# Kernel optimization log

Measured on AMD Instinct MI355X. Metric: run time of the kernel, lower is better.

The kernel has to match this reference:

```python
import jax, jax.numpy as jnp
import numpy as np

N_ANCHORS = 262144
N_GT = 100
IMG = 1024.0
N_SAMPLE = 256
POS_RATIO = 0.5
POS_T = 0.7
NEG_T = 0.3
ALLOWED_BORDER = 0.0
NUM_FG = int(POS_RATIO * N_SAMPLE)  # 128


def compute_overlap(a, g):
    """IoU between anchors a:(N,4) and gt g:(R,4), py-faster-rcnn +1 pixel convention."""
    area_a = (a[:, 2] - a[:, 0] + 1.0) * (a[:, 3] - a[:, 1] + 1.0)          # (N,)
    area_g = (g[:, 2] - g[:, 0] + 1.0) * (g[:, 3] - g[:, 1] + 1.0)          # (R,)
    iw = jnp.minimum(a[:, None, 2], g[None, :, 2]) - jnp.maximum(a[:, None, 0], g[None, :, 0]) + 1.0
    ih = jnp.minimum(a[:, None, 3], g[None, :, 3]) - jnp.maximum(a[:, None, 1], g[None, :, 1]) + 1.0
    inter = jnp.maximum(iw, 0.0) * jnp.maximum(ih, 0.0)                     # (N,R)
    return inter / (area_a[:, None] + area_g[None, :] - inter)


def bbox_transform(gt, an):
    """Encode gt boxes relative to anchors -> (dx,dy,dw,dh), shape (N,4)."""
    aw = an[:, 2] - an[:, 0] + 1.0
    ah = an[:, 3] - an[:, 1] + 1.0
    acx = an[:, 0] + 0.5 * aw
    acy = an[:, 1] + 0.5 * ah
    gw = gt[:, 2] - gt[:, 0] + 1.0
    gh = gt[:, 3] - gt[:, 1] + 1.0
    gcx = gt[:, 0] + 0.5 * gw
    gcy = gt[:, 1] + 0.5 * gh
    return jnp.stack([(gcx - acx) / aw, (gcy - acy) / ah,
                      jnp.log(gw / aw), jnp.log(gh / ah)], axis=1)


def keep_at_most(mask, k, key):
    """Keep at most k True entries of mask, chosen uniformly at random (fixed shape)."""
    r = jnp.where(mask, jax.random.uniform(key, mask.shape), jnp.inf)
    rank = jnp.argsort(jnp.argsort(r))  # rank[i] = position of i in ascending sort
    return mask & (rank < k)


def anchor_target(anchors, image_shape, gt, key):
    # anchors: (N,4), gt: (R,4)
    R = gt.shape[0]
    inside = ((anchors[:, 0] >= -ALLOWED_BORDER) & (anchors[:, 1] >= -ALLOWED_BORDER)
              & (anchors[:, 2] < ALLOWED_BORDER + image_shape[1])
              & (anchors[:, 3] < ALLOWED_BORDER + image_shape[0]))            # (N,)
    iou = compute_overlap(anchors, gt)                                        # (N,R)
    iou_m = jnp.where(inside[:, None], iou, -1.0)  # restrict to inside anchors
    max_ov = jnp.max(iou_m, axis=1)                                           # (N,)

    k1, k2, k3 = jax.random.split(key, 3)
    labels = jnp.full(anchors.shape[:1], -1.0, dtype=jnp.float32)
    # clobber_positives=False: background first
    labels = jnp.where(inside & (max_ov < NEG_T), 0.0, labels)
    # per-gt argmax anchors (tie set), randomly truncated to at most R like tf.random_shuffle[:R]
    gt_max = jnp.max(iou_m, axis=0)                                           # (R,)
    cand = jnp.any(iou_m == gt_max[None, :], axis=1) & inside                 # (N,)
    cand = keep_at_most(cand, R, k1)
    labels = jnp.where(cand, 1.0, labels)
    labels = jnp.where(inside & (max_ov >= POS_T), 1.0, labels)

    # balance: subsample positives to NUM_FG
    fg = labels == 1.0
    labels = jnp.where(fg & ~keep_at_most(fg, NUM_FG, k2), -1.0, labels)
    # subsample negatives to n_sample - n_fg
    n_fg = jnp.sum(labels == 1.0)
    bg = labels == 0.0
    labels = jnp.where(bg & ~keep_at_most(bg, N_SAMPLE - n_fg, k3), -1.0, labels)
    # umap: outside anchors stay -1
    labels = jnp.where(inside, labels, -1.0)

    # bbox targets: faithful to original tf.gather(gt, to_int32(max_overlaps))
    idx = jnp.clip(max_ov.astype(jnp.int32), 0, R - 1)
    tgt = bbox_transform(gt[idx], anchors)                                    # (N,4)
    tgt = jnp.where(inside[:, None], tgt, 0.0)  # scatter_nd at inside indices
    return labels[None], tgt[None]


def setup_inputs() -> dict:
    key = jax.random.key(0)
    k1, k2, k3, k4 = jax.random.split(key, 4)
    ctr = jax.random.uniform(k1, (N_ANCHORS, 2), minval=-64.0, maxval=IMG + 64.0)
    wh = jax.random.uniform(k2, (N_ANCHORS, 2), minval=16.0, maxval=256.0)
    anchors = jnp.concatenate([ctr - 0.5 * wh, ctr + 0.5 * wh], axis=1)
    gctr = jax.random.uniform(k3, (N_GT, 2), minval=100.0, maxval=IMG - 100.0)
    gwh = jax.random.uniform(k4, (N_GT, 2), minval=30.0, maxval=200.0)
    gt = jnp.concatenate([gctr - 0.5 * gwh, gctr + 0.5 * gwh], axis=1)
    return {"total_anchors": anchors[None],
            "image_shape": jnp.array([IMG, IMG], jnp.float32),
            "gt_boxes": gt[None]}


def reference(total_anchors, image_shape, gt_boxes):
    key = jax.random.key(42)  # original uses unseeded tf.random_shuffle
    labels, bbox_reg_targets = anchor_target(total_anchors[0], image_shape,
                                             gt_boxes[0][:, :4], key)
    return labels, bbox_reg_targets
```

## Files before the change

### kernel.cpp

```cpp
#include <hip/hip_runtime.h>
#include <stdint.h>

#define NGT_MAX 128
#define CAND_CAP 8192
#define CSEL_CAP 512
#define FILT_CAP 16384
#define SUB_CAP 2048


__host__ __device__ inline void tf2x32(uint32_t k0, uint32_t k1, uint32_t c0, uint32_t c1,
                                       uint32_t& o0, uint32_t& o1) {
  uint32_t ks[3] = {k0, k1, k0 ^ k1 ^ 0x1BD11BDAu};
  uint32_t x0 = c0 + ks[0];
  uint32_t x1 = c1 + ks[1];
  const int rot[2][4] = {{13, 15, 26, 6}, {17, 29, 16, 24}};
#pragma unroll
  for (int i = 0; i < 5; ++i) {
#pragma unroll
    for (int j = 0; j < 4; ++j) {
      x0 += x1;
      int r = rot[i & 1][j];
      x1 = (x1 << r) | (x1 >> (32 - r));
      x1 ^= x0;
    }
    x0 += ks[(i + 1) % 3];
    x1 += ks[(i + 2) % 3] + (uint32_t)(i + 1);
  }
  o0 = x0; o1 = x1;
}

__device__ inline uint64_t sel_key(uint32_t i, uint32_t ka, uint32_t kb) {
  uint32_t o0, o1;
  tf2x32(ka, kb, 0u, i, o0, o1);
  uint32_t bits = o0 ^ o1;
  return ((uint64_t)(bits >> 9) << 32) | (uint64_t)i;
}

__device__ inline uint32_t fmap(float v) {
  uint32_t u = __float_as_uint(v);
  return (u & 0x80000000u) ? ~u : (u | 0x80000000u);
}
__device__ inline float funmap(uint32_t m) {
  return (m & 0x80000000u) ? __uint_as_float(m & 0x7FFFFFFFu) : __uint_as_float(~m);
}

__device__ inline void cons_meta(uint32_t baseF, uint32_t baseB, uint32_t* needF,
                                 uint32_t* Tf, uint32_t* needB, uint32_t* Tb) {
  *needF = (baseF > 128u) ? 1u : 0u;
  uint64_t tf = 0, tb = 0;
  if (*needF) {
    tf = (((uint64_t)(128u * 32u)) << 23) / (uint64_t)baseF;
    if (tf > (1u << 23)) tf = (1u << 23);
  }
  uint32_t nfgmin = baseF < 128u ? baseF : 128u;
  uint32_t kbgmax = 256u - nfgmin;
  *needB = (baseB > 8192u + kbgmax) ? 1u : 0u;
  if (*needB) {
    tb = (((uint64_t)(kbgmax * 32u)) << 23) / (uint64_t)(baseB - 8192u);
    if (tb > (1u << 23)) tb = (1u << 23);
  }
  *Tf = (uint32_t)tf;
  *Tb = (uint32_t)tb;
}

__global__ void __launch_bounds__(256)
k_main(const float4* __restrict__ anc, const float* __restrict__ img,
       const float4* __restrict__ gt, int N, int R,
       uint32_t* __restrict__ pmax, uint32_t* __restrict__ gmaxu,
       float* __restrict__ LBL, float4* __restrict__ TGT,
       uint32_t* __restrict__ pmeta, uint32_t* __restrict__ counters) {
  __shared__ float4 sgt[NGT_MAX];
  __shared__ float sarea[NGT_MAX];
  __shared__ float sq[64 * 101];
  __shared__ uint32_t scnt[2];
  const int t = threadIdx.x, b = blockIdx.x;
  if (b == 0 && t < 16) counters[t] = 0u;
  if (t < 2) scnt[t] = 0u;
  if (t < R) {
    float4 g = gt[t];
    sgt[t] = g;
    {
#pragma clang fp contract(off)
      sarea[t] = (g.z - g.x + 1.0f) * (g.w - g.y + 1.0f);
    }
  }
  __syncthreads();
  const int lane = t & 63, lm = t & 3, q = t >> 2;
  const int i = b * 256 + t;
  const float H = img[0], W = img[1];
  float4 a = anc[i];
  bool inside = (a.x >= 0.0f) && (a.y >= 0.0f) && (a.z < W) && (a.w < H);
  float area_a;
  {
#pragma clang fp contract(off)
    area_a = (a.z - a.x + 1.0f) * (a.w - a.y + 1.0f);
  }
  if (!inside) area_a = __uint_as_float(0x7FC00000u);
  const bool b1 = (lm == 1), b2 = (lm == 2), b3 = (lm == 3);
  float part[25];
  float vmax = -1.0f;
#pragma unroll 4
  for (int s = 0; s < 25; ++s) {
    const int gb0 = 4 * s;
    if (gb0 >= R) break;
    float v2q[4];
#pragma unroll
    for (int k = 0; k < 4; ++k) {
      const int g = gb0 + k;
      if (g < R) {
        float4 gb = sgt[g];
        float v;
        {
#pragma clang fp contract(off)
          float iw = fminf(a.z, gb.z) - fmaxf(a.x, gb.x) + 1.0f;
          float ih = fminf(a.w, gb.w) - fmaxf(a.y, gb.y) + 1.0f;
          float inter = fmaxf(iw, 0.0f) * fmaxf(ih, 0.0f);
          v = inter / (area_a + sarea[g] - inter);
        }
        vmax = fmaxf(vmax, v);
        int s1 = __builtin_amdgcn_mov_dpp(__float_as_int(v), 0xB1, 0xF, 0xF, true);
        float v1 = fmaxf(v, __int_as_float(s1));
        int s2 = __builtin_amdgcn_mov_dpp(__float_as_int(v1), 0x4E, 0xF, 0xF, true);
        v2q[k] = fmaxf(v1, __int_as_float(s2));
      } else {
        v2q[k] = -1.0f;
      }
    }
    float p = v2q[0];
    p = b1 ? v2q[1] : p;
    p = b2 ? v2q[2] : p;
    p = b3 ? v2q[3] : p;
    part[s] = p;
  }
  float lbl = -1.0f;
  if (inside) {
    if (vmax < 0.3f) lbl = 0.0f;
    if (vmax >= 0.7f) lbl = 1.0f;
  }
  LBL[i] = lbl;
  unsigned long long bf = __ballot(lbl == 1.0f);
  unsigned long long bb = __ballot(lbl == 0.0f);
  if (lane == 0) {
    atomicAdd(&scnt[0], (uint32_t)__popcll(bf));
    atomicAdd(&scnt[1], (uint32_t)__popcll(bb));
  }
  float4 o = make_float4(0.f, 0.f, 0.f, 0.f);
  if (inside) {
    int idx = (int)vmax;
    idx = idx < 0 ? 0 : (idx > R - 1 ? R - 1 : idx);
    float4 gb = sgt[idx];
    {
#pragma clang fp contract(off)
      float aw = a.z - a.x + 1.0f;
      float ah = a.w - a.y + 1.0f;
      float acx = a.x + 0.5f * aw;
      float acy = a.y + 0.5f * ah;
      float gw = gb.z - gb.x + 1.0f;
      float gh = gb.w - gb.y + 1.0f;
      float gcx = gb.x + 0.5f * gw;
      float gcy = gb.y + 0.5f * gh;
      o.x = (gcx - acx) / aw;
      o.y = (gcy - acy) / ah;
      o.z = logf(gw / aw);
      o.w = logf(gh / ah);
    }
  }
  TGT[i] = o;
#pragma unroll
  for (int s = 0; s < 25; ++s) {
    const int g = 4 * s + lm;
    if (4 * s >= R) break;
    if (g < R) sq[q * 101 + g] = part[s];
  }
  __syncthreads();
  if (t < R) {
    float m = -1.0f;
#pragma unroll 8
    for (int k2 = 0; k2 < 64; ++k2) m = fmaxf(m, sq[k2 * 101 + t]);
    uint32_t u = fmap(m);
    pmax[b * R + t] = u;
    if (u > gmaxu[t]) atomicMax(&gmaxu[t], u);
  }
  if (t == 0) pmeta[b] = scnt[0] | (scnt[1] << 16);
}

__global__ void __launch_bounds__(256)
k_gather(const float4* __restrict__ anc, const float* __restrict__ img,
         const float4* __restrict__ gt, int N, int NB, int R,
         const uint32_t* __restrict__ pmax, const uint32_t* __restrict__ gmaxu,
         const uint32_t* __restrict__ pmeta,
         float* __restrict__ LBL,
         uint64_t* __restrict__ candList, uint32_t* __restrict__ candLbl,
         uint64_t* __restrict__ listF, uint64_t* __restrict__ listB,
         uint32_t* __restrict__ counters,
         uint32_t k1a, uint32_t k1b, uint32_t k2a, uint32_t k2b,
         uint32_t k3a, uint32_t k3b) {
  __shared__ uint64_t red[256];
  __shared__ int tg[NGT_MAX];
  __shared__ float tgm[NGT_MAX];
  __shared__ uint64_t cbuf[256];
  __shared__ uint32_t cbufL[256];
  __shared__ uint64_t bufF[256], bufB[256];
  __shared__ uint32_t cC, cF, cB, oC, oF, oB;
  __shared__ int tcnt;
  const int t = threadIdx.x, b = blockIdx.x;
  if (t == 0) { tcnt = 0; cC = 0u; cF = 0u; cB = 0u; }
  uint64_t sm = 0;
  for (int j = t; j < NB; j += 256) {
    uint32_t v = pmeta[j];
    sm += (uint64_t)(v & 0xFFFFu) | ((uint64_t)(v >> 16) << 32);
  }
  red[t] = sm;
  __syncthreads();
  for (int s = 128; s > 0; s >>= 1) {
    if (t < s) red[t] += red[t + s];
    __syncthreads();
  }
  const uint32_t baseF = (uint32_t)(red[0] & 0xFFFFFFFFu);
  const uint32_t baseB = (uint32_t)(red[0] >> 32);
  uint32_t needF, Tf, needB, Tb;
  cons_meta(baseF, baseB, &needF, &Tf, &needB, &Tb);
  if (t < R) {
    uint32_t pm = pmax[b * R + t];
    uint32_t gm = gmaxu[t];
    if (pm == gm) { int p = atomicAdd(&tcnt, 1); tg[p] = t; tgm[p] = funmap(gm); }
  }
  __syncthreads();
  const int C0 = tcnt;
  const int i = b * 256 + t;
  float old = LBL[i];
  bool isc = false;
  if (C0 > 0) {
    const float H = img[0], W = img[1];
    float4 a = anc[i];
    bool inside = (a.x >= 0.0f) && (a.y >= 0.0f) && (a.z < W) && (a.w < H);
    if (inside) {
      float area_a;
      {
#pragma clang fp contract(off)
        area_a = (a.z - a.x + 1.0f) * (a.w - a.y + 1.0f);
      }
      for (int j = 0; j < C0; ++j) {
        float4 gb = gt[tg[j]];
        float v;
        {
#pragma clang fp contract(off)
          float ag = (gb.z - gb.x + 1.0f) * (gb.w - gb.y + 1.0f);
          float iw = fminf(a.z, gb.z) - fmaxf(a.x, gb.x) + 1.0f;
          float ih = fminf(a.w, gb.w) - fmaxf(a.y, gb.y) + 1.0f;
          float inter = fmaxf(iw, 0.0f) * fmaxf(ih, 0.0f);
          v = inter / (area_a + ag - inter);
        }
        isc = isc || (v == tgm[j]);
      }
    }
  }
  if (isc) {
    uint32_t code = (old == 1.0f) ? 2u : ((old == 0.0f) ? 1u : 0u);
    uint32_t p = atomicAdd(&cC, 1u);
    cbuf[p] = sel_key((uint32_t)i, k1a, k1b);
    cbufL[p] = code;
  }
  float l1 = isc ? 1.0f : old;
  float out = l1;
  if (l1 == 1.0f) {
    uint64_t key = sel_key((uint32_t)i, k2a, k2b);
    if (needF && (uint32_t)(key >> 32) >= Tf) {
      out = -1.0f;
    } else {
      uint32_t p = atomicAdd(&cF, 1u);
      bufF[p] = key;
    }
  } else if (l1 == 0.0f) {
    uint64_t key = sel_key((uint32_t)i, k3a, k3b);
    if (needB && (uint32_t)(key >> 32) >= Tb) {
      out = -1.0f;
    } else {
      uint32_t p = atomicAdd(&cB, 1u);
      bufB[p] = key;
    }
  }
  LBL[i] = out;
  __syncthreads();
  if (t == 0 && cC) oC = atomicAdd(&counters[0], cC);
  if (t == 64 && cF) oF = atomicAdd(&counters[4], cF);
  if (t == 128 && cB) oB = atomicAdd(&counters[5], cB);
  __syncthreads();
  for (uint32_t j = t; j < cC; j += 256) {
    uint32_t p = oC + j;
    if (p < CAND_CAP) { candList[p] = cbuf[j]; candLbl[p] = cbufL[j]; }
  }
  for (uint32_t j = t; j < cF; j += 256) {
    uint32_t p = oF + j;
    if (p < FILT_CAP) listF[p] = bufF[j];
  }
  for (uint32_t j = t; j < cB; j += 256) {
    uint32_t p = oB + j;
    if (p < FILT_CAP) listB[p] = bufB[j];
  }
}

__device__ __forceinline__ void do_select(const uint64_t* list, uint32_t Mf, uint32_t k,
                                          uint32_t T, float* LBL, uint32_t* h,
                                          uint32_t* c0, uint32_t* c1, uint64_t* sub,
                                          uint32_t* scal, const uint32_t* drop,
                                          uint32_t nd) {
  const int t = threadIdx.x;
  if (Mf <= k) return;
  int bl = (T > 1u) ? (32 - __clz(T - 1u)) : 0;
  int shift = bl > 8 ? bl - 8 : 0;
  h[t] = 0u;
  if (t == 0) { scal[0] = 0u; scal[1] = 0u; scal[2] = 0u; }
  __syncthreads();
  for (uint32_t j = t; j < Mf; j += 256) {
    uint64_t key = list[j];
    bool skip = false;
    for (uint32_t d = 0; d < nd; ++d) skip = skip || (drop[d] == (uint32_t)key);
    if (!skip) atomicAdd(&h[((uint32_t)(key >> 32)) >> shift], 1u);
  }
  __syncthreads();
  c0[t] = h[t];
  __syncthreads();
  uint32_t* s = c0;
  uint32_t* d2 = c1;
  for (int dd = 1; dd < 256; dd <<= 1) {
    uint32_t v = s[t];
    if (t >= dd) v += s[t - dd];
    d2[t] = v;
    __syncthreads();
    uint32_t* tmp = s; s = d2; d2 = tmp;
  }
  uint32_t inc = s[t];
  uint32_t exc = inc - h[t];
  if (exc < k && inc >= k) { scal[1] = (uint32_t)t; scal[2] = k - exc; }
  __syncthreads();
  const uint32_t binb = scal[1], rneed = scal[2];
  for (uint32_t j = t; j < Mf; j += 256) {
    uint64_t key = list[j];
    bool skip = false;
    for (uint32_t d = 0; d < nd; ++d) skip = skip || (drop[d] == (uint32_t)key);
    if (skip) continue;
    uint32_t bin = ((uint32_t)(key >> 32)) >> shift;
    if (bin > binb) {
      LBL[(uint32_t)key] = -1.0f;
    } else if (bin == binb) {
      uint32_t p = atomicAdd(&scal[0], 1u);
      if (p < SUB_CAP) sub[p] = key;
    }
  }
  __syncthreads();
  uint32_t c = scal[0] < SUB_CAP ? scal[0] : SUB_CAP;
  for (uint32_t s2 = t; s2 < c; s2 += 256) {
    uint64_t key = sub[s2];
    uint32_t rank = 0u;
    for (uint32_t j = 0; j < c; ++j) rank += (sub[j] < key) ? 1u : 0u;
    if (rank >= rneed) LBL[(uint32_t)key] = -1.0f;
  }
  __syncthreads();
}

__global__ void __launch_bounds__(256)
k_sel(float* __restrict__ LBL, uint64_t* __restrict__ listF,
      uint64_t* __restrict__ listB, const uint64_t* __restrict__ candList,
      const uint32_t* __restrict__ candLbl, const uint32_t* __restrict__ pmeta,
      uint32_t* __restrict__ counters, int NB, int R,
      uint32_t k3a, uint32_t k3b) {
  __shared__ uint64_t red[256];
  __shared__ uint64_t ck[CSEL_CAP];
  __shared__ uint32_t cc[CSEL_CAP];
  __shared__ uint32_t drop[256];
  __shared__ uint32_t h[256], c0s[256], c1s[256];
  __shared__ uint64_t sub[SUB_CAP];
  __shared__ uint32_t scal[8];
  const int t = threadIdx.x;
  uint64_t sm = 0;
  for (int j = t; j < NB; j += 256) {
    uint32_t v = pmeta[j];
    sm += (uint64_t)(v & 0xFFFFu) | ((uint64_t)(v >> 16) << 32);
  }
  red[t] = sm;
  if (t < 8) scal[t] = 0u;
  uint32_t C = counters[0];
  if (C > CSEL_CAP) C = CSEL_CAP;
  for (uint32_t s = t; s < C; s += 256) { ck[s] = candList[s]; cc[s] = candLbl[s]; }
  __syncthreads();
  for (int s = 128; s > 0; s >>= 1) {
    if (t < s) red[t] += red[t + s];
    __syncthreads();
  }
  const uint32_t baseF = (uint32_t)(red[0] & 0xFFFFFFFFu);
  const uint32_t baseB = (uint32_t)(red[0] >> 32);
  uint32_t needFc, TfC, needBc, TbC;
  cons_meta(baseF, baseB, &needFc, &TfC, &needBc, &TbC);
  const uint32_t MfB0 = counters[5] < FILT_CAP ? counters[5] : FILT_CAP;
  for (uint32_t e = t; e < C; e += 256) {
    uint64_t key = ck[e];
    bool keep = true;
    if (C > (uint32_t)R) {
      uint32_t rank = 0;
      for (uint32_t j = 0; j < C; ++j) rank += (ck[j] < key) ? 1u : 0u;
      keep = (rank < (uint32_t)R);
    }
    uint32_t code = cc[e];
    uint32_t idx = (uint32_t)key;
    if (keep) {
      if (code != 2u) atomicAdd(&scal[4], 1u);
      if (code == 1u) atomicAdd(&scal[5], 1u);
    } else if (code != 2u) {
      uint32_t p = atomicAdd(&scal[3], 1u);
      if (p < 256) drop[p] = idx;
      if (code == 0u) {
        LBL[idx] = -1.0f;
      } else {
        uint64_t key3 = sel_key(idx, k3a, k3b);
        if (needBc && (uint32_t)(key3 >> 32) >= TbC) {
          LBL[idx] = -1.0f;
        } else {
          uint32_t qq = atomicAdd(&scal[6], 1u);
          if (MfB0 + qq < FILT_CAP) listB[MfB0 + qq] = key3;
          LBL[idx] = 0.0f;
        }
      }
    }
  }
  __syncthreads();
  const uint32_t fgflips = scal[4], bgflips = scal[5];
  const uint32_t nDrop = scal[3] < 256u ? scal[3] : 256u;
  const uint32_t nAdd = scal[6];
  const uint32_t M1 = baseF + fgflips;
  const uint32_t M2 = baseB - bgflips;
  const uint32_t nfg = M1 < 128u ? M1 : 128u;
  const uint32_t kbg = 256u - nfg;
  if (M1 > 128u) {
    uint32_t MfF = counters[4] < FILT_CAP ? counters[4] : FILT_CAP;
    uint32_t TF = needFc ? TfC : (1u << 23);
    do_select(listF, MfF, 128u, TF, LBL, h, c0s, c1s, sub, scal, drop, nDrop);
  }
  if (M2 > kbg) {
    uint32_t MfB = MfB0 + nAdd;
    if (MfB > FILT_CAP) MfB = FILT_CAP;
    uint32_t TB = needBc ? TbC : (1u << 23);
    do_select(listB, MfB, kbg, TB, LBL, h, c0s, c1s, sub, scal, drop, 0u);
  }
}

extern "C" void kernel_launch(void* const* d_in, const int* in_sizes, int n_in,
                              void* d_out, int out_size, void* d_ws, size_t ws_size,
                              hipStream_t stream) {
  (void)n_in; (void)out_size; (void)ws_size;
  const int N = in_sizes[0] / 4;
  const int R = in_sizes[2] / 4;
  const int NB = N / 256;
  const float4* anc = (const float4*)d_in[0];
  const float* img = (const float*)d_in[1];
  const float4* gtb = (const float4*)d_in[2];
  float* LBL = (float*)d_out;
  float4* TGT = (float4*)((float*)d_out + N);

  uint8_t* ws = (uint8_t*)d_ws;
  uint32_t* counters = (uint32_t*)ws;
  uint32_t* gmaxu = (uint32_t*)(ws + 512);
  uint32_t* pmeta = (uint32_t*)(ws + 1024);
  uint32_t* candLbl = (uint32_t*)(ws + 1024 + 4096);
  uint32_t* pmax = (uint32_t*)(ws + 65536);
  size_t off = 65536 + (size_t)NB * R * 4;
  off = (off + 7) & ~(size_t)7;
  uint64_t* candList = (uint64_t*)(ws + off);
  uint64_t* listF = (uint64_t*)(ws + off + CAND_CAP * 8);
  uint64_t* listB = (uint64_t*)(ws + off + CAND_CAP * 8 + FILT_CAP * 8);

  uint32_t k1a, k1b, k2a, k2b, k3a, k3b;
  tf2x32(0u, 42u, 0u, 0u, k1a, k1b);
  tf2x32(0u, 42u, 0u, 1u, k2a, k2b);
  tf2x32(0u, 42u, 0u, 2u, k3a, k3b);

  k_main<<<NB, 256, 0, stream>>>(anc, img, gtb, N, R, pmax, gmaxu, LBL, TGT, pmeta,
                                 counters);
  k_gather<<<NB, 256, 0, stream>>>(anc, img, gtb, N, NB, R, pmax, gmaxu, pmeta, LBL,
                                   candList, candLbl, listF, listB, counters,
                                   k1a, k1b, k2a, k2b, k3a, k3b);
  k_sel<<<1, 256, 0, stream>>>(LBL, listF, listB, candList, candLbl, pmeta, counters,
                               NB, R, k3a, k3b);
}
```

Baseline: 136.8 us.

## Split GT boxes across wavefront halves and reduce column maxima with DPP

k_main now gives each anchor two lanes, each scoring half of the GT boxes (50 each). This doubles the block count and halves the per-thread IoU loop and register array. The per-anchor max is merged with a cross-half shuffle, and the per-GT column max is pre-reduced across 16 lanes with DPP row shifts before going to a smaller shared buffer. k_gather now combines two pmax rows per block. The trade-off is a grid twice as large, more pmax partials to write, and a more delicate lane mapping.

```diff
diff --git a/kernel.cpp b/kernel.cpp
--- a/kernel.cpp
+++ b/kernel.cpp
@@ -63,6 +63,28 @@
   *Tb = (uint32_t)tb;
 }
 
+__device__ __forceinline__ float iou_ref(const float4& a, float area_a, const float4& gb,
+                                         float area_g) {
+#pragma clang fp contract(off)
+  float iw = fminf(a.z, gb.z) - fmaxf(a.x, gb.x) + 1.0f;
+  float ih = fminf(a.w, gb.w) - fmaxf(a.y, gb.y) + 1.0f;
+  float inter = fmaxf(iw, 0.0f) * fmaxf(ih, 0.0f);
+  return inter / (area_a + area_g - inter);
+}
+
+__device__ __forceinline__ float4 tgt_ref(const float4& a, const float4& gb) {
+#pragma clang fp contract(off)
+  float aw = a.z - a.x + 1.0f;
+  float ah = a.w - a.y + 1.0f;
+  float acx = a.x + 0.5f * aw;
+  float acy = a.y + 0.5f * ah;
+  float gw = gb.z - gb.x + 1.0f;
+  float gh = gb.w - gb.y + 1.0f;
+  float gcx = gb.x + 0.5f * gw;
+  float gcy = gb.y + 0.5f * gh;
+  return make_float4((gcx - acx) / aw, (gcy - acy) / ah, logf(gw / aw), logf(gh / ah));
+}
+
 __global__ void __launch_bounds__(256)
 k_main(const float4* __restrict__ anc, const float* __restrict__ img,
        const float4* __restrict__ gt, int N, int R,
@@ -71,7 +93,7 @@
        uint32_t* __restrict__ pmeta, uint32_t* __restrict__ counters) {
   __shared__ float4 sgt[NGT_MAX];
   __shared__ float sarea[NGT_MAX];
-  __shared__ float sq[64 * 101];
+  __shared__ float sq[16 * 101];
   __shared__ uint32_t scnt[2];
   const int t = threadIdx.x, b = blockIdx.x;
   if (b == 0 && t < 16) counters[t] = 0u;
@@ -84,9 +106,15 @@
       sarea[t] = (g.z - g.x + 1.0f) * (g.w - g.y + 1.0f);
     }
   }
-  __syncthreads();
-  const int lane = t & 63, lm = t & 3, q = t >> 2;
-  const int i = b * 256 + t;
+  for (int j = t; j < 16 * 101; j += 256) sq[j] = -1.0f;
+  __syncthreads();
+  const int lane = t & 63, wid = t >> 6;
+  const int h = lane >> 5;
+  const int al = lane & 31;
+  const int p = lane & 3;
+  const int i = b * 128 + wid * 32 + al;
+  const int gbase = 50 * h;
+  const int Rh = R - gbase;
   const float H = img[0], W = img[1];
   float4 a = anc[i];
   bool inside = (a.x >= 0.0f) && (a.y >= 0.0f) && (a.z < W) && (a.w < H);
@@ -96,87 +124,78 @@
     area_a = (a.z - a.x + 1.0f) * (a.w - a.y + 1.0f);
   }
   if (!inside) area_a = __uint_as_float(0x7FC00000u);
-  const bool b1 = (lm == 1), b2 = (lm == 2), b3 = (lm == 3);
-  float part[25];
+  const bool b1 = (p == 1), b2 = (p == 2), b3 = (p == 3);
+  float part[13];
   float vmax = -1.0f;
-#pragma unroll 4
-  for (int s = 0; s < 25; ++s) {
-    const int gb0 = 4 * s;
-    if (gb0 >= R) break;
+#pragma unroll
+  for (int s = 0; s < 13; ++s) {
     float v2q[4];
 #pragma unroll
     for (int k = 0; k < 4; ++k) {
-      const int g = gb0 + k;
-      if (g < R) {
+      const int j = 4 * s + k;
+      if (j < 50 && j < Rh) {
+        const int g = gbase + j;
         float4 gb = sgt[g];
-        float v;
-        {
-#pragma clang fp contract(off)
-          float iw = fminf(a.z, gb.z) - fmaxf(a.x, gb.x) + 1.0f;
-          float ih = fminf(a.w, gb.w) - fmaxf(a.y, gb.y) + 1.0f;
-          float inter = fmaxf(iw, 0.0f) * fmaxf(ih, 0.0f);
-          v = inter / (area_a + sarea[g] - inter);
-        }
+        float v = iou_ref(a, area_a, gb, sarea[g]);
         vmax = fmaxf(vmax, v);
-        int s1 = __builtin_amdgcn_mov_dpp(__float_as_int(v), 0xB1, 0xF, 0xF, true);
-        float v1 = fmaxf(v, __int_as_float(s1));
-        int s2 = __builtin_amdgcn_mov_dpp(__float_as_int(v1), 0x4E, 0xF, 0xF, true);
-        v2q[k] = fmaxf(v1, __int_as_float(s2));
+        int d1 = __builtin_amdgcn_mov_dpp(__float_as_int(v), 0xB1, 0xF, 0xF, true);
+        float v1 = fmaxf(v, __int_as_float(d1));
+        int d2 = __builtin_amdgcn_mov_dpp(__float_as_int(v1), 0x4E, 0xF, 0xF, true);
+        v2q[k] = fmaxf(v1, __int_as_float(d2));
       } else {
         v2q[k] = -1.0f;
       }
     }
-    float p = v2q[0];
-    p = b1 ? v2q[1] : p;
-    p = b2 ? v2q[2] : p;
-    p = b3 ? v2q[3] : p;
-    part[s] = p;
-  }
+    float pp = v2q[0];
+    pp = b1 ? v2q[1] : pp;
+    pp = b2 ? v2q[2] : pp;
+    pp = b3 ? v2q[3] : pp;
+    part[s] = pp;
+  }
+  vmax = fmaxf(vmax, __shfl_xor(vmax, 32));
   float lbl = -1.0f;
   if (inside) {
     if (vmax < 0.3f) lbl = 0.0f;
     if (vmax >= 0.7f) lbl = 1.0f;
   }
-  LBL[i] = lbl;
-  unsigned long long bf = __ballot(lbl == 1.0f);
-  unsigned long long bb = __ballot(lbl == 0.0f);
+  unsigned long long bf = __ballot(lbl == 1.0f) & 0xFFFFFFFFull;
+  unsigned long long bb = __ballot(lbl == 0.0f) & 0xFFFFFFFFull;
   if (lane == 0) {
     atomicAdd(&scnt[0], (uint32_t)__popcll(bf));
     atomicAdd(&scnt[1], (uint32_t)__popcll(bb));
   }
-  float4 o = make_float4(0.f, 0.f, 0.f, 0.f);
-  if (inside) {
-    int idx = (int)vmax;
-    idx = idx < 0 ? 0 : (idx > R - 1 ? R - 1 : idx);
-    float4 gb = sgt[idx];
-    {
-#pragma clang fp contract(off)
-      float aw = a.z - a.x + 1.0f;
-      float ah = a.w - a.y + 1.0f;
-      float acx = a.x + 0.5f * aw;
-      float acy = a.y + 0.5f * ah;
-      float gw = gb.z - gb.x + 1.0f;
-      float gh = gb.w - gb.y + 1.0f;
-      float gcx = gb.x + 0.5f * gw;
-      float gcy = gb.y + 0.5f * gh;
-      o.x = (gcx - acx) / aw;
-      o.y = (gcy - acy) / ah;
-      o.z = logf(gw / aw);
-      o.w = logf(gh / ah);
-    }
-  }
-  TGT[i] = o;
+  if (h == 0) {
+    LBL[i] = lbl;
+    float4 o = make_float4(0.f, 0.f, 0.f, 0.f);
+    if (inside) {
+      int idx = (int)vmax;
+      idx = idx < 0 ? 0 : (idx > R - 1 ? R - 1 : idx);
+      o = tgt_ref(a, sgt[idx]);
+    }
+    TGT[i] = o;
+  }
 #pragma unroll
-  for (int s = 0; s < 25; ++s) {
-    const int g = 4 * s + lm;
-    if (4 * s >= R) break;
-    if (g < R) sq[q * 101 + g] = part[s];
+  for (int s = 0; s < 13; ++s) {
+    float v = part[s];
+    int x = __builtin_amdgcn_mov_dpp(__float_as_int(v), 0x114, 0xF, 0xF, true);
+    v = fmaxf(v, __int_as_float(x));
+    x = __builtin_amdgcn_mov_dpp(__float_as_int(v), 0x118, 0xF, 0xF, true);
+    v = fmaxf(v, __int_as_float(x));
+    part[s] = v;
+  }
+  const int r = t >> 4;
+  if ((t & 15) >= 12) {
+#pragma unroll
+    for (int s = 0; s < 13; ++s) {
+      const int j = 4 * s + p;
+      if (j < 50 && j < Rh) sq[r * 101 + gbase + j] = part[s];
+    }
   }
   __syncthreads();
   if (t < R) {
     float m = -1.0f;
 #pragma unroll 8
-    for (int k2 = 0; k2 < 64; ++k2) m = fmaxf(m, sq[k2 * 101 + t]);
+    for (int r2 = 0; r2 < 16; ++r2) m = fmaxf(m, sq[r2 * 101 + t]);
     uint32_t u = fmap(m);
     pmax[b * R + t] = u;
     if (u > gmaxu[t]) atomicMax(&gmaxu[t], u);
@@ -186,7 +205,7 @@
 
 __global__ void __launch_bounds__(256)
 k_gather(const float4* __restrict__ anc, const float* __restrict__ img,
-         const float4* __restrict__ gt, int N, int NB, int R,
+         const float4* __restrict__ gt, int N, int NBm, int R,
          const uint32_t* __restrict__ pmax, const uint32_t* __restrict__ gmaxu,
          const uint32_t* __restrict__ pmeta,
          float* __restrict__ LBL,
@@ -206,7 +225,7 @@
   const int t = threadIdx.x, b = blockIdx.x;
   if (t == 0) { tcnt = 0; cC = 0u; cF = 0u; cB = 0u; }
   uint64_t sm = 0;
-  for (int j = t; j < NB; j += 256) {
+  for (int j = t; j < NBm; j += 256) {
     uint32_t v = pmeta[j];
     sm += (uint64_t)(v & 0xFFFFu) | ((uint64_t)(v >> 16) << 32);
   }
@@ -221,9 +240,14 @@
   uint32_t needF, Tf, needB, Tb;
   cons_meta(baseF, baseB, &needF, &Tf, &needB, &Tb);
   if (t < R) {
-    uint32_t pm = pmax[b * R + t];
     uint32_t gm = gmaxu[t];
-    if (pm == gm) { int p = atomicAdd(&tcnt, 1); tg[p] = t; tgm[p] = funmap(gm); }
+    uint32_t pm0 = pmax[(2 * b) * R + t];
+    uint32_t pm1 = pmax[(2 * b + 1) * R + t];
+    if (pm0 == gm || pm1 == gm) {
+      int pp = atomicAdd(&tcnt, 1);
+      tg[pp] = t;
+      tgm[pp] = funmap(gm);
+    }
   }
   __syncthreads();
   const int C0 = tcnt;
@@ -242,24 +266,21 @@
       }
       for (int j = 0; j < C0; ++j) {
         float4 gb = gt[tg[j]];
-        float v;
+        float ag;
         {
 #pragma clang fp contract(off)
-          float ag = (gb.z - gb.x + 1.0f) * (gb.w - gb.y + 1.0f);
-          float iw = fminf(a.z, gb.z) - fmaxf(a.x, gb.x) + 1.0f;
-          float ih = fminf(a.w, gb.w) - fmaxf(a.y, gb.y) + 1.0f;
-          float inter = fmaxf(iw, 0.0f) * fmaxf(ih, 0.0f);
-          v = inter / (area_a + ag - inter);
+          ag = (gb.z - gb.x + 1.0f) * (gb.w - gb.y + 1.0f);
         }
+        float v = iou_ref(a, area_a, gb, ag);
         isc = isc || (v == tgm[j]);
       }
     }
   }
   if (isc) {
     uint32_t code = (old == 1.0f) ? 2u : ((old == 0.0f) ? 1u : 0u);
-    uint32_t p = atomicAdd(&cC, 1u);
-    cbuf[p] = sel_key((uint32_t)i, k1a, k1b);
-    cbufL[p] = code;
+    uint32_t pp = atomicAdd(&cC, 1u);
+    cbuf[pp] = sel_key((uint32_t)i, k1a, k1b);
+    cbufL[pp] = code;
   }
   float l1 = isc ? 1.0f : old;
   float out = l1;
@@ -268,16 +289,16 @@
     if (needF && (uint32_t)(key >> 32) >= Tf) {
       out = -1.0f;
     } else {
-      uint32_t p = atomicAdd(&cF, 1u);
-      bufF[p] = key;
+      uint32_t pp = atomicAdd(&cF, 1u);
+      bufF[pp] = key;
     }
   } else if (l1 == 0.0f) {
     uint64_t key = sel_key((uint32_t)i, k3a, k3b);
     if (needB && (uint32_t)(key >> 32) >= Tb) {
       out = -1.0f;
     } else {
-      uint32_t p = atomicAdd(&cB, 1u);
-      bufB[p] = key;
+      uint32_t pp = atomicAdd(&cB, 1u);
+      bufB[pp] = key;
     }
   }
   LBL[i] = out;
@@ -287,16 +308,16 @@
   if (t == 128 && cB) oB = atomicAdd(&counters[5], cB);
   __syncthreads();
   for (uint32_t j = t; j < cC; j += 256) {
-    uint32_t p = oC + j;
-    if (p < CAND_CAP) { candList[p] = cbuf[j]; candLbl[p] = cbufL[j]; }
+    uint32_t pp = oC + j;
+    if (pp < CAND_CAP) { candList[pp] = cbuf[j]; candLbl[pp] = cbufL[j]; }
   }
   for (uint32_t j = t; j < cF; j += 256) {
-    uint32_t p = oF + j;
-    if (p < FILT_CAP) listF[p] = bufF[j];
+    uint32_t pp = oF + j;
+    if (pp < FILT_CAP) listF[pp] = bufF[j];
   }
   for (uint32_t j = t; j < cB; j += 256) {
-    uint32_t p = oB + j;
-    if (p < FILT_CAP) listB[p] = bufB[j];
+    uint32_t pp = oB + j;
+    if (pp < FILT_CAP) listB[pp] = bufB[j];
   }
 }
 
@@ -344,8 +365,8 @@
     if (bin > binb) {
       LBL[(uint32_t)key] = -1.0f;
     } else if (bin == binb) {
-      uint32_t p = atomicAdd(&scal[0], 1u);
-      if (p < SUB_CAP) sub[p] = key;
+      uint32_t pp = atomicAdd(&scal[0], 1u);
+      if (pp < SUB_CAP) sub[pp] = key;
     }
   }
   __syncthreads();
@@ -363,7 +384,7 @@
 k_sel(float* __restrict__ LBL, uint64_t* __restrict__ listF,
       uint64_t* __restrict__ listB, const uint64_t* __restrict__ candList,
       const uint32_t* __restrict__ candLbl, const uint32_t* __restrict__ pmeta,
-      uint32_t* __restrict__ counters, int NB, int R,
+      uint32_t* __restrict__ counters, int NBm, int R,
       uint32_t k3a, uint32_t k3b) {
   __shared__ uint64_t red[256];
   __shared__ uint64_t ck[CSEL_CAP];
@@ -374,7 +395,7 @@
   __shared__ uint32_t scal[8];
   const int t = threadIdx.x;
   uint64_t sm = 0;
-  for (int j = t; j < NB; j += 256) {
+  for (int j = t; j < NBm; j += 256) {
     uint32_t v = pmeta[j];
     sm += (uint64_t)(v & 0xFFFFu) | ((uint64_t)(v >> 16) << 32);
   }
@@ -407,8 +428,8 @@
       if (code != 2u) atomicAdd(&scal[4], 1u);
       if (code == 1u) atomicAdd(&scal[5], 1u);
     } else if (code != 2u) {
-      uint32_t p = atomicAdd(&scal[3], 1u);
-      if (p < 256) drop[p] = idx;
+      uint32_t pp = atomicAdd(&scal[3], 1u);
+      if (pp < 256) drop[pp] = idx;
       if (code == 0u) {
         LBL[idx] = -1.0f;
       } else {
@@ -450,7 +471,8 @@
   (void)n_in; (void)out_size; (void)ws_size;
   const int N = in_sizes[0] / 4;
   const int R = in_sizes[2] / 4;
-  const int NB = N / 256;
+  const int NBm = N / 128;
+  const int NBg = N / 256;
   const float4* anc = (const float4*)d_in[0];
   const float* img = (const float*)d_in[1];
   const float4* gtb = (const float4*)d_in[2];
@@ -461,9 +483,9 @@
   uint32_t* counters = (uint32_t*)ws;
   uint32_t* gmaxu = (uint32_t*)(ws + 512);
   uint32_t* pmeta = (uint32_t*)(ws + 1024);
-  uint32_t* candLbl = (uint32_t*)(ws + 1024 + 4096);
+  uint32_t* candLbl = (uint32_t*)(ws + 16384);
   uint32_t* pmax = (uint32_t*)(ws + 65536);
-  size_t off = 65536 + (size_t)NB * R * 4;
+  size_t off = 65536 + (size_t)NBm * R * 4;
   off = (off + 7) & ~(size_t)7;
   uint64_t* candList = (uint64_t*)(ws + off);
   uint64_t* listF = (uint64_t*)(ws + off + CAND_CAP * 8);
@@ -474,11 +496,11 @@
   tf2x32(0u, 42u, 0u, 1u, k2a, k2b);
   tf2x32(0u, 42u, 0u, 2u, k3a, k3b);
 
-  k_main<<<NB, 256, 0, stream>>>(anc, img, gtb, N, R, pmax, gmaxu, LBL, TGT, pmeta,
-                                 counters);
-  k_gather<<<NB, 256, 0, stream>>>(anc, img, gtb, N, NB, R, pmax, gmaxu, pmeta, LBL,
-                                   candList, candLbl, listF, listB, counters,
-                                   k1a, k1b, k2a, k2b, k3a, k3b);
+  k_main<<<NBm, 256, 0, stream>>>(anc, img, gtb, N, R, pmax, gmaxu, LBL, TGT, pmeta,
+                                  counters);
+  k_gather<<<NBg, 256, 0, stream>>>(anc, img, gtb, N, NBm, R, pmax, gmaxu, pmeta, LBL,
+                                    candList, candLbl, listF, listB, counters,
+                                    k1a, k1b, k2a, k2b, k3a, k3b);
   k_sel<<<1, 256, 0, stream>>>(LBL, listF, listB, candList, candLbl, pmeta, counters,
-                               NB, R, k3a, k3b);
-}
+                               NBm, R, k3a, k3b);
+}
```

After: 136.5 us. No clear change (-0.2%).
